# Performance work log

Hardware: AMD Instinct MI355X
Metric: run time of the kernel (lower is better)

## Reference

```python
import jax, jax.numpy as jnp
import numpy as np

B, L, H, T = 128, 512, 512, 24
START, STOP = T - 2, T - 1
NEG = -10000.0


def setup_inputs() -> dict:
    key = jax.random.key(0)
    k1, k2, k3, k4 = jax.random.split(key, 4)
    features = jax.random.normal(k1, (B, L, H), dtype=jnp.float32)
    emission_w = jax.random.normal(k2, (T, H), dtype=jnp.float32) * 0.02
    emission_b = jnp.zeros((T,), dtype=jnp.float32)
    transitions = jax.random.normal(k3, (T, T), dtype=jnp.float32)
    # CRF constraints: nothing transitions INTO START; nothing transitions OUT of STOP
    # (transitions[i, j] = score of transitioning j -> i, per the forward_alg indexing)
    transitions = transitions.at[START, :].set(NEG).at[:, STOP].set(NEG)
    lengths = jax.random.randint(k4, (B,), 1, L + 1)
    return {"features": features, "emission_w": emission_w,
            "emission_b": emission_b, "transitions": transitions,
            "lengths": lengths}


def reference(features, emission_w, emission_b, transitions, lengths):
    # emission scores: [B, L, T]
    emit = jnp.einsum('blh,th->blt', features, emission_w) + emission_b
    Bn, Ln, Tn = emit.shape
    # init alphas: -10000 everywhere except START tag
    fv0 = jnp.full((Bn, Tn), NEG, dtype=emit.dtype).at[:, START].set(0.0)

    def step(fv, xs):
        e_t, t = xs  # e_t: [B, T], t: scalar timestep
        # tag_var[b, j, k] = emit[b, j] + transitions[j, k] + fv[b, k]
        scores = e_t[:, :, None] + transitions[None, :, :] + fv[:, None, :]
        new = jax.nn.logsumexp(scores, axis=2)  # [B, T]
        # only advance sequences that haven't ended (equivalent to gathering
        # forward_var at index lengths[b] in the original)
        fv = jnp.where((t < lengths)[:, None], new, fv)
        return fv, None

    fv, _ = jax.lax.scan(step, fv0, (jnp.swapaxes(emit, 0, 1), jnp.arange(Ln)))
    terminal = fv + transitions[STOP][None, :]
    return jax.nn.logsumexp(terminal, axis=1)  # alpha: [B]
```

## Files before the change

kernel.cpp:

```cpp
#include <hip/hip_runtime.h>
#include <hip/hip_bf16.h>

typedef unsigned int uint;
typedef unsigned short ushort;

#define Bn 128
#define Ln 512
#define Hn 512
#define Tn 24
#define START_TAG 22
#define STOP_TAG 23
#define NCH 32
#define CHL 16

using frag_ab = __attribute__((ext_vector_type(8))) short;
using frag_cd = __attribute__((ext_vector_type(4))) float;
union ABU { frag_ab f; uint u[4]; };

#define PACKW(x, y) \
  __builtin_amdgcn_perm(__float_as_uint(y), __float_as_uint(x), 0x07060302u)
#define MFMA16 __builtin_amdgcn_mfma_f32_16x16x32_bf16

__device__ __forceinline__ float bf2f(ushort v) {
  return __uint_as_float(((uint)v) << 16);
}
__device__ __forceinline__ ushort f2bf_rne(float x) {
  uint u = __float_as_uint(x);
  return (ushort)((u + 0x7FFFu + ((u >> 16) & 1u)) >> 16);
}
__device__ __forceinline__ float rlf(float v, int l) {
  return __int_as_float(__builtin_amdgcn_readlane(__float_as_int(v), l));
}
__device__ __forceinline__ float rfl(float v) {
  return __int_as_float(__builtin_amdgcn_readfirstlane(__float_as_int(v)));
}
__device__ __forceinline__ uint bperm(int addr, uint v) {
  return (uint)__builtin_amdgcn_ds_bpermute(addr, (int)v);
}

__global__ __launch_bounds__(256) void wconv(const float* __restrict__ W,
                                             ushort* __restrict__ Wbf) {
  int i = blockIdx.x * 256 + threadIdx.x;
  if (i < Tn * Hn) Wbf[i] = f2bf_rne(W[i]);
}

__global__ __launch_bounds__(256, 4) void fused_kernel(
    const float* __restrict__ feat, const ushort* __restrict__ Wbf,
    const float* __restrict__ bias, const float* __restrict__ trans,
    const int* __restrict__ lengths, ushort* __restrict__ G,
    float* __restrict__ Rc, float* __restrict__ u0buf) {
  __shared__ float ee[4][CHL][32];
  const int wv = threadIdx.x >> 6, l = threadIdx.x & 63;
  const int ct = l & 15, g = l >> 4;
  const int chunk = blockIdx.x * 4 + wv;
  const int b = chunk >> 5, c = chunk & 31;

  const float* fp = feat + (size_t)(chunk * CHL + ct) * Hn + 8 * g;
  const ushort* wp0 = Wbf + ct * Hn + 8 * g;
  const ushort* wp1 = Wbf + (16 + (ct & 7)) * Hn + 8 * g;
  frag_cd acc0 = {0.f, 0.f, 0.f, 0.f}, acc1 = {0.f, 0.f, 0.f, 0.f};
#pragma unroll 4
  for (int kk = 0; kk < 16; ++kk) {
    float4 fa = *(const float4*)(fp + kk * 32);
    float4 fb = *(const float4*)(fp + kk * 32 + 4);
    frag_ab b0 = *(const frag_ab*)(wp0 + kk * 32);
    frag_ab b1 = *(const frag_ab*)(wp1 + kk * 32);
    ABU A;
    A.u[0] = PACKW(fa.x, fa.y);
    A.u[1] = PACKW(fa.z, fa.w);
    A.u[2] = PACKW(fb.x, fb.y);
    A.u[3] = PACKW(fb.z, fb.w);
    acc0 = MFMA16(A.f, b0, acc0, 0, 0, 0);
    acc1 = MFMA16(A.f, b1, acc1, 0, 0, 0);
  }
  const float bs0 = bias[ct];
  const float bs1 = bias[16 + (ct & 7)];
#pragma unroll
  for (int r = 0; r < 4; ++r) {
    ee[wv][4 * g + r][ct] = __expf(acc0[r] + bs0);
    if (ct < 8) {
      ee[wv][4 * g + r][16 + ct] = __expf(acc1[r] + bs1);
      ee[wv][4 * g + r][24 + ct] = 0.f;
    }
  }
  __syncthreads();
  if (c == 0 && l < Tn) u0buf[b * Tn + l] = ee[wv][0][l];

  ABU A0c, A1c;
#pragma unroll
  for (int h = 0; h < 4; ++h) {
    int k0 = 8 * g + 2 * h, k1 = k0 + 1;
    float e00 = (k0 < Tn) ? __expf(trans[ct * Tn + k0]) : 0.f;
    float e01 = (k1 < Tn) ? __expf(trans[ct * Tn + k1]) : 0.f;
    A0c.u[h] = PACKW(e00, e01);
    float e10 = (k0 < Tn && ct < 8) ? __expf(trans[(16 + ct) * Tn + k0]) : 0.f;
    float e11 = (k1 < Tn && ct < 8) ? __expf(trans[(16 + ct) * Tn + k1]) : 0.f;
    A1c.u[h] = PACKW(e10, e11);
  }

  const int len = lengths[b];
  const int lo = (c == 0) ? 1 : 0;
  int hi = len - c * CHL;
  if (hi > CHL) hi = CHL;

  frag_cd D00, D01, D10, D11;
#pragma unroll
  for (int r = 0; r < 4; ++r) {
    float dv = (4 * g + r == ct) ? 1.f : 0.f;
    D00[r] = dv; D11[r] = dv; D01[r] = 0.f; D10[r] = 0.f;
  }

  float R = 0.f;
  const int addr0 = (ct + 32 * (g & 1)) * 4;
  const int addr1 = addr0 + 64;
  const bool mhi = (g >= 2);

#define RENORMF()                                                       \
  do {                                                                  \
    float ref = fmaxf(fmaxf(D00[0], D00[1]), fmaxf(D00[2], D00[3]));    \
    ref = rfl(ref);                                                     \
    int ebx = ((__float_as_int(ref) >> 23) & 255) - 127;                \
    float sc = __int_as_float((uint)(127 - ebx) << 23);                 \
    _Pragma("unroll") for (int r = 0; r < 4; ++r) {                     \
      D00[r] *= sc; D01[r] *= sc; D10[r] *= sc; D11[r] *= sc;           \
    }                                                                   \
    R += (float)ebx * 0.6931471805599453f;                              \
  } while (0)

  int stepc = 0;
  for (int lt = lo; lt < hi; ++lt) {
    uint p000 = PACKW(D00[0], D00[1]), p001 = PACKW(D00[2], D00[3]);
    uint p010 = PACKW(D01[0], D01[1]), p011 = PACKW(D01[2], D01[3]);
    uint p100 = PACKW(D10[0], D10[1]), p101 = PACKW(D10[2], D10[3]);
    uint p110 = PACKW(D11[0], D11[1]), p111 = PACKW(D11[2], D11[3]);
    ABU Bf0, Bf1;
    {
      uint a0 = bperm(addr0, p000), b0 = bperm(addr0, p100);
      uint a1 = bperm(addr0, p001), b1 = bperm(addr0, p101);
      uint a2 = bperm(addr1, p000), b2 = bperm(addr1, p100);
      uint a3 = bperm(addr1, p001), b3 = bperm(addr1, p101);
      Bf0.u[0] = mhi ? b0 : a0;
      Bf0.u[1] = mhi ? b1 : a1;
      Bf0.u[2] = mhi ? b2 : a2;
      Bf0.u[3] = mhi ? b3 : a3;
      a0 = bperm(addr0, p010); b0 = bperm(addr0, p110);
      a1 = bperm(addr0, p011); b1 = bperm(addr0, p111);
      a2 = bperm(addr1, p010); b2 = bperm(addr1, p110);
      a3 = bperm(addr1, p011); b3 = bperm(addr1, p111);
      Bf1.u[0] = mhi ? b0 : a0;
      Bf1.u[1] = mhi ? b1 : a1;
      Bf1.u[2] = mhi ? b2 : a2;
      Bf1.u[3] = mhi ? b3 : a3;
    }
    frag_cd z = {0.f, 0.f, 0.f, 0.f};
    frag_cd N00 = MFMA16(A0c.f, Bf0.f, z, 0, 0, 0);
    frag_cd N01 = MFMA16(A0c.f, Bf1.f, z, 0, 0, 0);
    frag_cd N10 = MFMA16(A1c.f, Bf0.f, z, 0, 0, 0);
    frag_cd N11 = MFMA16(A1c.f, Bf1.f, z, 0, 0, 0);
    float4 s0 = *(const float4*)(&ee[wv][lt][4 * g]);
    float4 s1 = *(const float4*)(&ee[wv][lt][16 + 4 * g]);
    D00[0] = N00[0] * s0.x; D00[1] = N00[1] * s0.y;
    D00[2] = N00[2] * s0.z; D00[3] = N00[3] * s0.w;
    D01[0] = N01[0] * s0.x; D01[1] = N01[1] * s0.y;
    D01[2] = N01[2] * s0.z; D01[3] = N01[3] * s0.w;
    D10[0] = N10[0] * s1.x; D10[1] = N10[1] * s1.y;
    D10[2] = N10[2] * s1.z; D10[3] = N10[3] * s1.w;
    D11[0] = N11[0] * s1.x; D11[1] = N11[1] * s1.y;
    D11[2] = N11[2] * s1.z; D11[3] = N11[3] * s1.w;
    if ((++stepc & 3) == 0) RENORMF();
  }
  RENORMF();

  ushort* Gc = G + (size_t)chunk * 1024;
  uint2 w2;
  w2.x = PACKW(D00[0], D00[1]); w2.y = PACKW(D00[2], D00[3]);
  *(uint2*)(Gc + ct * 32 + 4 * g) = w2;
  w2.x = PACKW(D01[0], D01[1]); w2.y = PACKW(D01[2], D01[3]);
  *(uint2*)(Gc + (16 + ct) * 32 + 4 * g) = w2;
  w2.x = PACKW(D10[0], D10[1]); w2.y = PACKW(D10[2], D10[3]);
  *(uint2*)(Gc + ct * 32 + 16 + 4 * g) = w2;
  w2.x = PACKW(D11[0], D11[1]); w2.y = PACKW(D11[2], D11[3]);
  *(uint2*)(Gc + (16 + ct) * 32 + 16 + 4 * g) = w2;
  if (l == 0) Rc[chunk] = R;
}

__global__ __launch_bounds__(64) void passB(
    const float* __restrict__ trans, const ushort* __restrict__ G,
    const float* __restrict__ Rc, const float* __restrict__ u0buf,
    float* __restrict__ out) {
  const int b = blockIdx.x;
  const int j = threadIdx.x;
  const bool act = j < Tn;
  const int jj = act ? j : 0;

  float v = act ? u0buf[b * Tn + jj] * __expf(trans[jj * Tn + START_TAG]) : 0.f;
  float R = 0.f;
  const ushort* Gb = G + (size_t)b * (NCH * 1024);

#pragma unroll 1
  for (int c = 0; c < NCH; ++c) {
    const ushort* Gc = Gb + c * 1024;
    float p[24];
#pragma unroll
    for (int k = 0; k < 24; ++k) p[k] = bf2f(Gc[k * 32 + jj]);
    float s = 0.f;
#pragma unroll
    for (int k = 0; k < 24; ++k) s = fmaf(p[k], rlf(v, k), s);
    v = act ? s : 0.f;
    R += Rc[b * NCH + c];
    float ref = rfl(v);
    int ebx = ((__float_as_int(ref) >> 23) & 255) - 127;
    v *= __int_as_float((uint)(127 - ebx) << 23);
    R += (float)ebx * 0.6931471805599453f;
  }

  float term = act ? v * __expf(trans[STOP_TAG * Tn + jj]) : 0.f;
  term += __shfl_xor(term, 1, 64);
  term += __shfl_xor(term, 2, 64);
  term += __shfl_xor(term, 4, 64);
  term += __shfl_xor(term, 8, 64);
  term += __shfl_xor(term, 16, 64);
  term += __shfl_xor(term, 32, 64);
  if (j == 0) out[b] = R + logf(term);
}

extern "C" void kernel_launch(void* const* d_in, const int* in_sizes, int n_in,
                              void* d_out, int out_size, void* d_ws,
                              size_t ws_size, hipStream_t stream) {
  const float* feat = (const float*)d_in[0];
  const float* W = (const float*)d_in[1];
  const float* bias = (const float*)d_in[2];
  const float* trans = (const float*)d_in[3];
  const int* lengths = (const int*)d_in[4];
  float* out = (float*)d_out;

  ushort* G = (ushort*)d_ws;
  float* Rc = (float*)((char*)d_ws + 8388608);
  float* u0buf = (float*)((char*)d_ws + 8404992);
  ushort* Wbf = (ushort*)((char*)d_ws + 8417280);

  wconv<<<48, 256, 0, stream>>>(W, Wbf);
  fused_kernel<<<Bn * NCH / 4, 256, 0, stream>>>(feat, Wbf, bias, trans,
                                                 lengths, G, Rc, u0buf);
  passB<<<Bn, 64, 0, stream>>>(trans, G, Rc, u0buf, out);
}
```

Measured before the change: 233.7 us.

## Split emission GEMM and chunk chain into separate kernels with prefetched bf16 emissions

The fused GEMM-plus-chain kernel is split into an emission kernel that writes exp(emissions) as bf16 to a workspace, and a chain kernel that reads them back. The chain loop is unrolled into groups of four steps with register-prefetched emission loads and a renormalisation per group, removing the shared-memory staging and block-wide barrier. The intent is to let the memory-bound GEMM and the latency-bound recurrence run at their own occupancy. In exchange it adds a kernel launch, a global round trip for the emissions, and extra bf16 rounding of the emission factors.

Result: no change. 234.7 us (+0.5%).

```diff
diff --git a/kernel.cpp b/kernel.cpp
--- a/kernel.cpp
+++ b/kernel.cpp
@@ -24,6 +24,12 @@
 __device__ __forceinline__ float bf2f(ushort v) {
   return __uint_as_float(((uint)v) << 16);
 }
+__device__ __forceinline__ float bflo(uint v) {
+  return __uint_as_float(v << 16);
+}
+__device__ __forceinline__ float bfhi(uint v) {
+  return __uint_as_float(v & 0xffff0000u);
+}
 __device__ __forceinline__ ushort f2bf_rne(float x) {
   uint u = __float_as_uint(x);
   return (ushort)((u + 0x7FFFu + ((u >> 16) & 1u)) >> 16);
@@ -44,20 +50,16 @@
   if (i < Tn * Hn) Wbf[i] = f2bf_rne(W[i]);
 }
 
-__global__ __launch_bounds__(256, 4) void fused_kernel(
+__global__ __launch_bounds__(256) void emit_kernel(
     const float* __restrict__ feat, const ushort* __restrict__ Wbf,
-    const float* __restrict__ bias, const float* __restrict__ trans,
-    const int* __restrict__ lengths, ushort* __restrict__ G,
-    float* __restrict__ Rc, float* __restrict__ u0buf) {
-  __shared__ float ee[4][CHL][32];
+    const float* __restrict__ bias, ushort* __restrict__ eemit) {
   const int wv = threadIdx.x >> 6, l = threadIdx.x & 63;
   const int ct = l & 15, g = l >> 4;
-  const int chunk = blockIdx.x * 4 + wv;
-  const int b = chunk >> 5, c = chunk & 31;
-
-  const float* fp = feat + (size_t)(chunk * CHL + ct) * Hn + 8 * g;
+  const int row0 = blockIdx.x * 64 + wv * 16;
+  const float* fp = feat + (size_t)(row0 + ct) * Hn + 8 * g;
   const ushort* wp0 = Wbf + ct * Hn + 8 * g;
   const ushort* wp1 = Wbf + (16 + (ct & 7)) * Hn + 8 * g;
+
   frag_cd acc0 = {0.f, 0.f, 0.f, 0.f}, acc1 = {0.f, 0.f, 0.f, 0.f};
 #pragma unroll 4
   for (int kk = 0; kk < 16; ++kk) {
@@ -73,18 +75,25 @@
     acc0 = MFMA16(A.f, b0, acc0, 0, 0, 0);
     acc1 = MFMA16(A.f, b1, acc1, 0, 0, 0);
   }
+
   const float bs0 = bias[ct];
   const float bs1 = bias[16 + (ct & 7)];
 #pragma unroll
   for (int r = 0; r < 4; ++r) {
-    ee[wv][4 * g + r][ct] = __expf(acc0[r] + bs0);
-    if (ct < 8) {
-      ee[wv][4 * g + r][16 + ct] = __expf(acc1[r] + bs1);
-      ee[wv][4 * g + r][24 + ct] = 0.f;
-    }
-  }
-  __syncthreads();
-  if (c == 0 && l < Tn) u0buf[b * Tn + l] = ee[wv][0][l];
+    size_t row = row0 + 4 * g + r;
+    eemit[row * Tn + ct] = f2bf_rne(__expf(acc0[r] + bs0));
+    if (ct < 8) eemit[row * Tn + 16 + ct] = f2bf_rne(__expf(acc1[r] + bs1));
+  }
+}
+
+__global__ __launch_bounds__(256) void chain_kernel(
+    const ushort* __restrict__ eemit, const float* __restrict__ trans,
+    const int* __restrict__ lengths, ushort* __restrict__ G,
+    float* __restrict__ Rc) {
+  const int wv = threadIdx.x >> 6, l = threadIdx.x & 63;
+  const int ct = l & 15, g = l >> 4;
+  const int chunk = blockIdx.x * 4 + wv;
+  const int b = chunk >> 5, c = chunk & 31;
 
   ABU A0c, A1c;
 #pragma unroll
@@ -114,6 +123,60 @@
   const int addr0 = (ct + 32 * (g & 1)) * 4;
   const int addr1 = addr0 + 64;
   const bool mhi = (g >= 2);
+  const bool g2 = (g < 2);
+  const ushort* e0p = eemit + (size_t)(b * Ln + c * CHL) * Tn + 4 * g;
+  const ushort* e1p = e0p + 16;
+  const uint2 zz = {0u, 0u};
+
+#define LD2(Z0, Z1, T)                                   \
+  do {                                                   \
+    Z0 = *(const uint2*)(e0p + (T) * Tn);                \
+    Z1 = g2 ? *(const uint2*)(e1p + (T) * Tn) : zz;      \
+  } while (0)
+
+#define STEP_CORE(Z0, Z1)                                                  \
+  do {                                                                     \
+    uint p000 = PACKW(D00[0], D00[1]), p001 = PACKW(D00[2], D00[3]);       \
+    uint p010 = PACKW(D01[0], D01[1]), p011 = PACKW(D01[2], D01[3]);       \
+    uint p100 = PACKW(D10[0], D10[1]), p101 = PACKW(D10[2], D10[3]);       \
+    uint p110 = PACKW(D11[0], D11[1]), p111 = PACKW(D11[2], D11[3]);       \
+    ABU Bf0, Bf1;                                                          \
+    {                                                                      \
+      uint a0 = bperm(addr0, p000), b0 = bperm(addr0, p100);               \
+      uint a1 = bperm(addr0, p001), b1 = bperm(addr0, p101);               \
+      uint a2 = bperm(addr1, p000), b2 = bperm(addr1, p100);               \
+      uint a3 = bperm(addr1, p001), b3 = bperm(addr1, p101);               \
+      Bf0.u[0] = mhi ? b0 : a0;                                            \
+      Bf0.u[1] = mhi ? b1 : a1;                                            \
+      Bf0.u[2] = mhi ? b2 : a2;                                            \
+      Bf0.u[3] = mhi ? b3 : a3;                                            \
+      a0 = bperm(addr0, p010); b0 = bperm(addr0, p110);                    \
+      a1 = bperm(addr0, p011); b1 = bperm(addr0, p111);                    \
+      a2 = bperm(addr1, p010); b2 = bperm(addr1, p110);                    \
+      a3 = bperm(addr1, p011); b3 = bperm(addr1, p111);                    \
+      Bf1.u[0] = mhi ? b0 : a0;                                            \
+      Bf1.u[1] = mhi ? b1 : a1;                                            \
+      Bf1.u[2] = mhi ? b2 : a2;                                            \
+      Bf1.u[3] = mhi ? b3 : a3;                                            \
+    }                                                                      \
+    frag_cd z_ = {0.f, 0.f, 0.f, 0.f};                                     \
+    frag_cd N00 = MFMA16(A0c.f, Bf0.f, z_, 0, 0, 0);                       \
+    frag_cd N01 = MFMA16(A0c.f, Bf1.f, z_, 0, 0, 0);                       \
+    frag_cd N10 = MFMA16(A1c.f, Bf0.f, z_, 0, 0, 0);                       \
+    frag_cd N11 = MFMA16(A1c.f, Bf1.f, z_, 0, 0, 0);                       \
+    float sx0 = bflo(Z0.x), sx1 = bfhi(Z0.x);                              \
+    float sx2 = bflo(Z0.y), sx3 = bfhi(Z0.y);                              \
+    float sy0 = bflo(Z1.x), sy1 = bfhi(Z1.x);                              \
+    float sy2 = bflo(Z1.y), sy3 = bfhi(Z1.y);                              \
+    D00[0] = N00[0] * sx0; D00[1] = N00[1] * sx1;                          \
+    D00[2] = N00[2] * sx2; D00[3] = N00[3] * sx3;                          \
+    D01[0] = N01[0] * sx0; D01[1] = N01[1] * sx1;                          \
+    D01[2] = N01[2] * sx2; D01[3] = N01[3] * sx3;                          \
+    D10[0] = N10[0] * sy0; D10[1] = N10[1] * sy1;                          \
+    D10[2] = N10[2] * sy2; D10[3] = N10[3] * sy3;                          \
+    D11[0] = N11[0] * sy0; D11[1] = N11[1] * sy1;                          \
+    D11[2] = N11[2] * sy2; D11[3] = N11[3] * sy3;                          \
+  } while (0)
 
 #define RENORMF()                                                       \
   do {                                                                  \
@@ -127,47 +190,40 @@
     R += (float)ebx * 0.6931471805599453f;                              \
   } while (0)
 
-  int stepc = 0;
-  for (int lt = lo; lt < hi; ++lt) {
-    uint p000 = PACKW(D00[0], D00[1]), p001 = PACKW(D00[2], D00[3]);
-    uint p010 = PACKW(D01[0], D01[1]), p011 = PACKW(D01[2], D01[3]);
-    uint p100 = PACKW(D10[0], D10[1]), p101 = PACKW(D10[2], D10[3]);
-    uint p110 = PACKW(D11[0], D11[1]), p111 = PACKW(D11[2], D11[3]);
-    ABU Bf0, Bf1;
-    {
-      uint a0 = bperm(addr0, p000), b0 = bperm(addr0, p100);
-      uint a1 = bperm(addr0, p001), b1 = bperm(addr0, p101);
-      uint a2 = bperm(addr1, p000), b2 = bperm(addr1, p100);
-      uint a3 = bperm(addr1, p001), b3 = bperm(addr1, p101);
-      Bf0.u[0] = mhi ? b0 : a0;
-      Bf0.u[1] = mhi ? b1 : a1;
-      Bf0.u[2] = mhi ? b2 : a2;
-      Bf0.u[3] = mhi ? b3 : a3;
-      a0 = bperm(addr0, p010); b0 = bperm(addr0, p110);
-      a1 = bperm(addr0, p011); b1 = bperm(addr0, p111);
-      a2 = bperm(addr1, p010); b2 = bperm(addr1, p110);
-      a3 = bperm(addr1, p011); b3 = bperm(addr1, p111);
-      Bf1.u[0] = mhi ? b0 : a0;
-      Bf1.u[1] = mhi ? b1 : a1;
-      Bf1.u[2] = mhi ? b2 : a2;
-      Bf1.u[3] = mhi ? b3 : a3;
+  uint2 za0, za1, zb0, zb1, zc0, zc1, zd0, zd1;
+  uint2 ya0, ya1, yb0, yb1, yc0, yc1, yd0, yd1;
+  LD2(za0, za1, 0); LD2(zb0, zb1, 1); LD2(zc0, zc1, 2); LD2(zd0, zd1, 3);
+
+#define DOGROUP(BASE)                                            \
+  do {                                                           \
+    if ((BASE) + 0 >= lo && (BASE) + 0 < hi) STEP_CORE(za0, za1);\
+    if ((BASE) + 1 >= lo && (BASE) + 1 < hi) STEP_CORE(zb0, zb1);\
+    if ((BASE) + 2 >= lo && (BASE) + 2 < hi) STEP_CORE(zc0, zc1);\
+    if ((BASE) + 3 >= lo && (BASE) + 3 < hi) STEP_CORE(zd0, zd1);\
+    RENORMF();                                                   \
+  } while (0)
+
+  if (hi > 0) {
+    LD2(ya0, ya1, 4); LD2(yb0, yb1, 5); LD2(yc0, yc1, 6); LD2(yd0, yd1, 7);
+    DOGROUP(0);
+    if (hi > 4) {
+      za0 = ya0; za1 = ya1; zb0 = yb0; zb1 = yb1;
+      zc0 = yc0; zc1 = yc1; zd0 = yd0; zd1 = yd1;
+      LD2(ya0, ya1, 8); LD2(yb0, yb1, 9); LD2(yc0, yc1, 10); LD2(yd0, yd1, 11);
+      DOGROUP(4);
+      if (hi > 8) {
+        za0 = ya0; za1 = ya1; zb0 = yb0; zb1 = yb1;
+        zc0 = yc0; zc1 = yc1; zd0 = yd0; zd1 = yd1;
+        LD2(ya0, ya1, 12); LD2(yb0, yb1, 13);
+        LD2(yc0, yc1, 14); LD2(yd0, yd1, 15);
+        DOGROUP(8);
+        if (hi > 12) {
+          za0 = ya0; za1 = ya1; zb0 = yb0; zb1 = yb1;
+          zc0 = yc0; zc1 = yc1; zd0 = yd0; zd1 = yd1;
+          DOGROUP(12);
+        }
+      }
     }
-    frag_cd z = {0.f, 0.f, 0.f, 0.f};
-    frag_cd N00 = MFMA16(A0c.f, Bf0.f, z, 0, 0, 0);
-    frag_cd N01 = MFMA16(A0c.f, Bf1.f, z, 0, 0, 0);
-    frag_cd N10 = MFMA16(A1c.f, Bf0.f, z, 0, 0, 0);
-    frag_cd N11 = MFMA16(A1c.f, Bf1.f, z, 0, 0, 0);
-    float4 s0 = *(const float4*)(&ee[wv][lt][4 * g]);
-    float4 s1 = *(const float4*)(&ee[wv][lt][16 + 4 * g]);
-    D00[0] = N00[0] * s0.x; D00[1] = N00[1] * s0.y;
-    D00[2] = N00[2] * s0.z; D00[3] = N00[3] * s0.w;
-    D01[0] = N01[0] * s0.x; D01[1] = N01[1] * s0.y;
-    D01[2] = N01[2] * s0.z; D01[3] = N01[3] * s0.w;
-    D10[0] = N10[0] * s1.x; D10[1] = N10[1] * s1.y;
-    D10[2] = N10[2] * s1.z; D10[3] = N10[3] * s1.w;
-    D11[0] = N11[0] * s1.x; D11[1] = N11[1] * s1.y;
-    D11[2] = N11[2] * s1.z; D11[3] = N11[3] * s1.w;
-    if ((++stepc & 3) == 0) RENORMF();
   }
   RENORMF();
 
@@ -186,14 +242,16 @@
 
 __global__ __launch_bounds__(64) void passB(
     const float* __restrict__ trans, const ushort* __restrict__ G,
-    const float* __restrict__ Rc, const float* __restrict__ u0buf,
+    const float* __restrict__ Rc, const ushort* __restrict__ eemit,
     float* __restrict__ out) {
   const int b = blockIdx.x;
   const int j = threadIdx.x;
   const bool act = j < Tn;
   const int jj = act ? j : 0;
 
-  float v = act ? u0buf[b * Tn + jj] * __expf(trans[jj * Tn + START_TAG]) : 0.f;
+  float v = act ? bf2f(eemit[(size_t)b * Ln * Tn + jj]) *
+                      __expf(trans[jj * Tn + START_TAG])
+                : 0.f;
   float R = 0.f;
   const ushort* Gb = G + (size_t)b * (NCH * 1024);
 
@@ -234,13 +292,13 @@
   const int* lengths = (const int*)d_in[4];
   float* out = (float*)d_out;
 
-  ushort* G = (ushort*)d_ws;
-  float* Rc = (float*)((char*)d_ws + 8388608);
-  float* u0buf = (float*)((char*)d_ws + 8404992);
-  ushort* Wbf = (ushort*)((char*)d_ws + 8417280);
+  ushort* eemit = (ushort*)d_ws;
+  ushort* G = (ushort*)((char*)d_ws + 3145728);
+  float* Rc = (float*)((char*)d_ws + 11534336);
+  ushort* Wbf = (ushort*)((char*)d_ws + 11550720);
 
   wconv<<<48, 256, 0, stream>>>(W, Wbf);
-  fused_kernel<<<Bn * NCH / 4, 256, 0, stream>>>(feat, Wbf, bias, trans,
-                                                 lengths, G, Rc, u0buf);
-  passB<<<Bn, 64, 0, stream>>>(trans, G, Rc, u0buf, out);
-}
+  emit_kernel<<<1024, 256, 0, stream>>>(feat, Wbf, bias, eemit);
+  chain_kernel<<<1024, 256, 0, stream>>>(eemit, trans, lengths, G, Rc);
+  passB<<<Bn, 64, 0, stream>>>(trans, G, Rc, eemit, out);
+}
```
